# Performance work log

Hardware: AMD Instinct MI355X
Metric: run time of the kernel (lower is better)

The kernel has to match this reference:

```python
import jax, jax.numpy as jnp
import numpy as np

B, NB, H, E, NCT, NL = 16, 4096, 128, 65536, 32, 2
LN_EPS = 1e-5


def _layernorm(x, scale, bias):
    mu = jnp.mean(x, axis=-1, keepdims=True)
    var = jnp.var(x, axis=-1, keepdims=True)
    return (x - mu) / jnp.sqrt(var + LN_EPS) * scale + bias


def setup_inputs() -> dict:
    key = jax.random.key(0)
    ks = jax.random.split(key, 18)
    s = 1.0 / np.sqrt(H)
    inp = {
        'block_tokens': jax.random.normal(ks[0], (B, NB, H), jnp.float32),
        'edge_structure': jnp.full((E,), 0.5, jnp.float32),
        'ct_emb': 0.1 * jax.random.normal(ks[1], (NCT, E), jnp.float32),
        'W_proj': s * jax.random.normal(ks[2], (H, H), jnp.float32),
        'b_proj': jnp.zeros((H,), jnp.float32),
        'W_gate': (1.0 / np.sqrt(2 * H)) * jax.random.normal(ks[3], (2 * H, H), jnp.float32),
        'b_gate': jnp.zeros((H,), jnp.float32),
        'ln_scale': jnp.ones((NL, H), jnp.float32),
        'ln_bias': jnp.zeros((NL, H), jnp.float32),
        'W1': s * jax.random.normal(ks[4], (NL, H, 2 * H), jnp.float32),
        'b1': jnp.zeros((NL, 2 * H), jnp.float32),
        'W2': (1.0 / np.sqrt(2 * H)) * jax.random.normal(ks[5], (NL, 2 * H, H), jnp.float32),
        'b2': jnp.zeros((NL, H), jnp.float32),
        'cancer_type': jax.random.randint(ks[6], (B,), 0, NCT),
        'edge_src': jax.random.randint(ks[7], (E,), 0, NB),
        'edge_dst': jax.random.randint(ks[8], (E,), 0, NB),
        'block_active': jax.random.bernoulli(ks[9], 0.9, (B, NB)),
    }
    return inp


def reference(block_tokens, edge_structure, ct_emb, W_proj, b_proj, W_gate, b_gate,
              ln_scale, ln_bias, W1, b1, W2, b2,
              cancer_type, edge_src, edge_dst, block_active):
    # per-edge signed weights, masked by active src/dst blocks  -> (B, E)
    structure = jax.nn.sigmoid(edge_structure)
    edge_w = structure[None, :] * ct_emb[cancer_type]
    edge_w = edge_w * block_active[:, edge_src].astype(edge_w.dtype) \
                    * block_active[:, edge_dst].astype(edge_w.dtype)
    # route projection + ELU
    h_route = jax.nn.elu(jnp.einsum('bnh,hd->bnd', block_tokens, W_proj) + b_proj)
    # gather sources, weight, scatter-add to destinations
    weighted = edge_w[..., None] * h_route[:, edge_src, :]          # (B, E, H)
    messages = jnp.zeros_like(block_tokens).at[:, edge_dst, :].add(weighted)
    # gated residual
    gate = jax.nn.sigmoid(
        jnp.einsum('bnh,hd->bnd', jnp.concatenate([block_tokens, messages], axis=-1), W_gate) + b_gate)
    x = block_tokens + gate * messages
    # norm + FFN layers (dropout is identity at inference)
    for l in range(NL):
        normed = _layernorm(x, ln_scale[l], ln_bias[l])
        h = jax.nn.elu(jnp.einsum('bnh,hf->bnf', normed, W1[l]) + b1[l])
        x = x + jnp.einsum('bnf,fh->bnh', h, W2[l]) + b2[l]
    return (x, edge_w)
```

## Files before the change

### kernel.cpp

```cpp
#include <hip/hip_runtime.h>
#include <hip/hip_bf16.h>

#define BB     16
#define NBLK   4096
#define HD     128
#define NE     65536
#define MTOT   (BB * NBLK)

typedef __attribute__((ext_vector_type(8))) short bf16x8;
typedef __attribute__((ext_vector_type(4))) float f32x4;

__device__ __forceinline__ float bf2f(unsigned short u) {
    union { unsigned int i; float f; } v; v.i = ((unsigned int)u) << 16; return v.f;
}
__device__ __forceinline__ unsigned short f2bf(float f) {
    __bf16 h = (__bf16)f;
    unsigned short u;
    __builtin_memcpy(&u, &h, 2);
    return u;
}
__device__ __forceinline__ float ldf(const void* p, size_t i, int f32m) {
    return f32m ? ((const float*)p)[i] : bf2f(((const unsigned short*)p)[i]);
}
__device__ __forceinline__ int get_active(const void* p, int i, int mode) {
    switch (mode) {
        case 1:  return ((const unsigned char*)p)[i] != 0;
        case 2:  return ((const unsigned short*)p)[i] != 0;
        case 3:  return ((const float*)p)[i] != 0.f;
        default: return ((const int*)p)[i] != 0;
    }
}
__device__ __forceinline__ float elu_f(float v) {
    const float e = __expf(v);
    return v > 0.f ? v : e - 1.f;
}
__device__ __forceinline__ float sig_f(float v) {
    return 1.f / (1.f + __expf(-v));
}

__global__ void probe_k(const unsigned int* __restrict__ es,
                        const unsigned int* __restrict__ act,
                        int* __restrict__ flags)
{
    const int lane = threadIdx.x;
    const unsigned int v0 = act[lane], v1 = act[64 + lane];
    auto le1  = [](unsigned int v) { return v <= 1u; };
    auto byt  = [](unsigned int v) {
        return ((v & 0xFFu) <= 1u) && (((v >> 8) & 0xFFu) <= 1u) &&
               (((v >> 16) & 0xFFu) <= 1u) && ((v >> 24) <= 1u); };
    auto f32b = [](unsigned int v) { return v == 0u || v == 0x3F800000u; };
    auto bfb  = [](unsigned int v) {
        unsigned short h0 = (unsigned short)(v & 0xFFFFu), h1 = (unsigned short)(v >> 16);
        return (h0 == 0u || h0 == 0x3F80u) && (h1 == 0u || h1 == 0x3F80u); };
    const unsigned long long m_le1 = __ballot(le1(v0) && le1(v1));
    const unsigned long long m_byt = __ballot(byt(v0) && byt(v1));
    const unsigned long long m_f32 = __ballot(f32b(v0) && f32b(v1));
    const unsigned long long m_bf  = __ballot(bfb(v0) && bfb(v1));
    if (lane == 0) {
        flags[0] = (es[0] != 0x3F003F00u) ? 1 : 0;
        const unsigned long long full = ~0ull;
        flags[1] = (m_le1 == full) ? 0
                 : (m_byt == full) ? 1
                 : (m_f32 == full) ? 3
                 : (m_bf  == full) ? 2 : 0;
    }
}

__global__ __launch_bounds__(256) void transpose_k(
    const void* p0, const void* p1, const void* p2, const void* p3,
    const void* p4, const void* p5, unsigned short* __restrict__ wsT,
    const int* __restrict__ flags)
{
    const void* srcs[6]  = {p0, p1, p2, p3, p4, p5};
    const int eoffs[6]   = {0, 0, 0, 32768, 0, 32768};
    const int Ks[6]      = {128, 256, 128, 128, 256, 256};
    const int nsh[6]     = {7,   7,   8,   8,   7,   7};
    const int offs[6]    = {0, 16384, 49152, 81920, 114688, 147456};
    const int f32m = flags[0];
    const int z = blockIdx.y;
    const int K = Ks[z];
    const int Nn = 1 << nsh[z];
    const int idx = blockIdx.x * 256 + threadIdx.x;
    if (idx >= K * Nn) return;
    const int k = idx >> nsh[z];
    const int n = idx & (Nn - 1);
    wsT[offs[z] + n * K + k] = f2bf(ldf(srcs[z], (size_t)eoffs[z] + idx, f32m));
}

__global__ __launch_bounds__(256) void csr_count_k(const int* __restrict__ edst,
                                                   int* __restrict__ cnt)
{
    const int e = blockIdx.x * 256 + threadIdx.x;
    atomicAdd(&cnt[edst[e]], 1);
}

__global__ __launch_bounds__(1024) void csr_scan_k(const int* __restrict__ cnt,
                                                   int* __restrict__ ofs,
                                                   int* __restrict__ cur)
{
    __shared__ int part[1024];
    const int t = threadIdx.x;
    const int4 c = ((const int4*)cnt)[t];
    part[t] = c.x + c.y + c.z + c.w;
    __syncthreads();
    #pragma unroll
    for (int off = 1; off < 1024; off <<= 1) {
        const int v = (t >= off) ? part[t - off] : 0;
        __syncthreads();
        part[t] += v;
        __syncthreads();
    }
    const int base = t ? part[t - 1] : 0;
    int4 o;
    o.x = base; o.y = o.x + c.x; o.z = o.y + c.y; o.w = o.z + c.z;
    ((int4*)ofs)[t] = o;
    ((int4*)cur)[t] = o;
    if (t == 1023) ofs[4096] = part[1023];
}

__global__ __launch_bounds__(256) void csr_fill_k(const int* __restrict__ edst,
                                                  int* __restrict__ cur,
                                                  int* __restrict__ eidx,
                                                  int* __restrict__ pos_e)
{
    const int e = blockIdx.x * 256 + threadIdx.x;
    const int pos = atomicAdd(&cur[edst[e]], 1);
    eidx[pos] = e;
    pos_e[e] = pos;
}

__global__ __launch_bounds__(256) void edge_k(
    const void* __restrict__ es, const void* __restrict__ ctE,
    const int* __restrict__ ctype, const int* __restrict__ esrc, const int* __restrict__ edst,
    const void* __restrict__ act, const int* __restrict__ pos_e,
    float* __restrict__ out_ew, float2* __restrict__ compact,
    const int* __restrict__ flags)
{
    const int f32m = flags[0], am = flags[1];
    const int idx = blockIdx.x * 256 + threadIdx.x;
    const int b = idx >> 16;
    const int e = idx & 65535;
    const int s = esrc[e];
    const float sv  = sig_f(ldf(es, e, f32m));
    const float emb = ldf(ctE, (size_t)ctype[b] * NE + e, f32m);
    const int a1 = get_active(act, b * NBLK + s, am);
    const int a2 = get_active(act, b * NBLK + edst[e], am);
    const float w = (a1 && a2) ? sv * emb : 0.f;
    out_ew[idx] = w;
    compact[((size_t)b << 16) + pos_e[e]] = make_float2(w, __int_as_float(s));
}

__global__ __launch_bounds__(256) void gather_k(
    const float2* __restrict__ compact, const int* __restrict__ ofs,
    const unsigned short* __restrict__ hr, unsigned short* __restrict__ msg)
{
    const int blk = blockIdx.x;
    const int xcd = blk & 7;
    const int i   = blk >> 3;
    const int b   = xcd * 2 + (i & 1);
    const int d   = ((i >> 1) << 2) | (threadIdx.x >> 6);
    const int lane = threadIdx.x & 63;
    const int sub  = lane >> 4;
    const int l15  = lane & 15;
    const int j1 = ofs[d + 1];
    const size_t bbase = (size_t)b * NBLK * HD;
    const float2* cb = compact + ((size_t)b << 16);
    float acc[8];
    #pragma unroll
    for (int i2 = 0; i2 < 8; ++i2) acc[i2] = 0.f;
    int j = ofs[d] + sub;
    float2 c = (j < j1) ? cb[j] : make_float2(0.f, 0.f);
    while (j < j1) {
        const int jn = j + 4;
        const float2 cn = (jn < j1) ? cb[jn] : make_float2(0.f, 0.f);
        if (c.x != 0.f) {
            const int src = __float_as_int(c.y);
            const bf16x8 v = *(const bf16x8*)(hr + bbase + (size_t)src * HD + l15 * 8);
            #pragma unroll
            for (int i2 = 0; i2 < 8; ++i2)
                acc[i2] += c.x * bf2f((unsigned short)v[i2]);
        }
        c = cn; j = jn;
    }
    #pragma unroll
    for (int i2 = 0; i2 < 8; ++i2) {
        acc[i2] += __shfl_xor(acc[i2], 16);
        acc[i2] += __shfl_xor(acc[i2], 32);
    }
    if (sub == 0) {
        bf16x8 o;
        #pragma unroll
        for (int i2 = 0; i2 < 8; ++i2) o[i2] = (short)f2bf(acc[i2]);
        *(bf16x8*)(msg + bbase + (size_t)d * HD + l15 * 8) = o;
    }
}

__global__ __launch_bounds__(256) void route_k(
    const void* __restrict__ bt,
    unsigned short* __restrict__ bt16,
    const unsigned short* __restrict__ WT,
    const void* __restrict__ bias,
    unsigned short* __restrict__ hr,
    const int* __restrict__ flags)
{
    constexpr int K = 128, N = 128, KI = 4, NTW = 2, TILES = 8, NBUF = 4;
    const int f32m = flags[0];
    const int t    = threadIdx.x;
    const int lane = t & 63;
    const int wave = t >> 6;
    const int q    = lane >> 4;
    const int l15  = lane & 15;
    const int n0   = wave * 32;

    {
        const size_t base = (size_t)blockIdx.x * (128 * HD);
        #pragma unroll
        for (int it = 0; it < 8; ++it) {
            const size_t i = base + (size_t)it * 2048 + (size_t)t * 8;
            if (f32m) {
                const float* qp = (const float*)bt + i;
                f32x4 lo = *(const f32x4*)qp;
                f32x4 hi = *(const f32x4*)(qp + 4);
                bf16x8 r;
                #pragma unroll
                for (int j = 0; j < 4; ++j) { r[j] = (short)f2bf(lo[j]); r[4 + j] = (short)f2bf(hi[j]); }
                *(bf16x8*)(bt16 + i) = r;
            } else {
                *(bf16x8*)(bt16 + i) = *(const bf16x8*)((const unsigned short*)bt + i);
            }
        }
    }

    bf16x8 Bf[KI][NTW];
    #pragma unroll
    for (int ki = 0; ki < KI; ++ki)
        #pragma unroll
        for (int nt = 0; nt < NTW; ++nt)
            Bf[ki][nt] = *(const bf16x8*)(WT + (size_t)(n0 + nt * 16 + l15) * K + ki * 32 + q * 8);
    float biasv[NTW];
    #pragma unroll
    for (int nt = 0; nt < NTW; ++nt)
        biasv[nt] = ldf(bias, n0 + nt * 16 + l15, f32m);

    const int tile0 = blockIdx.x * TILES;
    bf16x8 Af[NBUF][KI];
    auto loadA = [&](int tt) {
        const int arow = (tile0 + tt) * 16 + l15;
        if (f32m) {
            const float* ap = (const float*)bt + (size_t)arow * K;
            #pragma unroll
            for (int ki = 0; ki < KI; ++ki) {
                const int k = ki * 32 + q * 8;
                f32x4 a0 = *(const f32x4*)(ap + k);
                f32x4 a1 = *(const f32x4*)(ap + k + 4);
                bf16x8 r;
                #pragma unroll
                for (int j = 0; j < 4; ++j) { r[j] = (short)f2bf(a0[j]); r[4 + j] = (short)f2bf(a1[j]); }
                Af[tt % NBUF][ki] = r;
            }
        } else {
            const unsigned short* ap = (const unsigned short*)bt + (size_t)arow * K;
            #pragma unroll
            for (int ki = 0; ki < KI; ++ki)
                Af[tt % NBUF][ki] = *(const bf16x8*)(ap + ki * 32 + q * 8);
        }
    };
    #pragma unroll
    for (int p = 0; p < NBUF; ++p) loadA(p);

    #pragma unroll
    for (int tt = 0; tt < TILES; ++tt) {
        const int s = tt % NBUF;
        f32x4 acc[NTW];
        #pragma unroll
        for (int i = 0; i < NTW; ++i) acc[i] = (f32x4){0.f, 0.f, 0.f, 0.f};
        #pragma unroll
        for (int ki = 0; ki < KI; ++ki)
            #pragma unroll
            for (int nt = 0; nt < NTW; ++nt)
                acc[nt] = __builtin_amdgcn_mfma_f32_16x16x32_bf16(Af[s][ki], Bf[ki][nt], acc[nt], 0, 0, 0);

        if (tt + NBUF < TILES) loadA(tt + NBUF);

        const int m0 = (tile0 + tt) * 16;
        #pragma unroll
        for (int nt = 0; nt < NTW; ++nt) {
            #pragma unroll
            for (int r = 0; r < 4; ++r) {
                const int row = m0 + q * 4 + r;
                const int col = n0 + nt * 16 + l15;
                const float v = acc[nt][r] + biasv[nt];
                hr[(size_t)row * N + col] = f2bf(elu_f(v));
            }
        }
    }
}

#define XI(xt, row, col)      x_lds[xt][row][((col) + 4 * (row)) & 127]
#define UI(hf, tl, row, col)  U[hf][tl][row][((col) + 8 * (row)) & 255]

__global__ __launch_bounds__(512, 2) void mega_k(
    const unsigned short* __restrict__ bt16,
    const unsigned short* __restrict__ msg,
    const void* __restrict__ btf,
    const unsigned short* __restrict__ WT,
    const void* __restrict__ bg,
    const void* __restrict__ b1, const void* __restrict__ b2,
    const void* __restrict__ lns, const void* __restrict__ lnb,
    float* __restrict__ xout,
    const int* __restrict__ flags)
{
    __shared__ __align__(16) float          x_lds[4][32][128];
    __shared__ __align__(16) unsigned short U[2][2][32][256];

    const int f32m = flags[0];
    const int t    = threadIdx.x;
    const int lane = t & 63;
    const int wave = t >> 6;
    const int hf   = wave >> 2;
    const int wv   = wave & 3;
    const int q    = lane >> 4;
    const int l15  = lane & 15;
    const int rhf  = blockIdx.x * 128 + hf * 64;
    const int ng   = wv * 32;

    float          btv[2][2][2][4];
    unsigned short mgu[2][2][2][4];
    #pragma unroll
    for (int tl = 0; tl < 2; ++tl)
        #pragma unroll
        for (int tt = 0; tt < 2; ++tt)
            #pragma unroll
            for (int nt = 0; nt < 2; ++nt)
                #pragma unroll
                for (int r = 0; r < 4; ++r) {
                    const size_t gi = (size_t)(rhf + tl * 32 + tt * 16 + q * 4 + r) * HD
                                      + ng + nt * 16 + l15;
                    btv[tl][tt][nt][r] = ldf(btf, gi, f32m);
                    mgu[tl][tt][nt][r] = msg[gi];
                }

    const unsigned short* WgT = WT + 16384;

    bf16x8 Bg[8][2];
    #pragma unroll
    for (int ki = 0; ki < 8; ++ki)
        #pragma unroll
        for (int nt = 0; nt < 2; ++nt)
            Bg[ki][nt] = *(const bf16x8*)(WgT + (size_t)(ng + nt * 16 + l15) * 256 + ki * 32 + q * 8);
    float biasg[2];
    #pragma unroll
    for (int nt = 0; nt < 2; ++nt) biasg[nt] = ldf(bg, ng + nt * 16 + l15, f32m);

    #pragma unroll
    for (int tl = 0; tl < 2; ++tl) {
        const int xt = hf * 2 + tl;
        bf16x8 Ag[2][8];
        #pragma unroll
        for (int tt = 0; tt < 2; ++tt) {
            const int arow = rhf + tl * 32 + tt * 16 + l15;
            #pragma unroll
            for (int ki = 0; ki < 8; ++ki) {
                const int k = ki * 32 + q * 8;
                Ag[tt][ki] = (k < HD)
                    ? *(const bf16x8*)(bt16 + (size_t)arow * HD + k)
                    : *(const bf16x8*)(msg  + (size_t)arow * HD + (k - HD));
            }
        }
        #pragma unroll
        for (int tt = 0; tt < 2; ++tt) {
            f32x4 acc[2];
            #pragma unroll
            for (int nt = 0; nt < 2; ++nt) acc[nt] = (f32x4){0.f, 0.f, 0.f, 0.f};
            __builtin_amdgcn_s_setprio(1);
            #pragma unroll
            for (int ki = 0; ki < 8; ++ki)
                #pragma unroll
                for (int nt = 0; nt < 2; ++nt)
                    acc[nt] = __builtin_amdgcn_mfma_f32_16x16x32_bf16(Ag[tt][ki], Bg[ki][nt], acc[nt], 0, 0, 0);
            __builtin_amdgcn_s_setprio(0);
            #pragma unroll
            for (int nt = 0; nt < 2; ++nt)
                #pragma unroll
                for (int r = 0; r < 4; ++r) {
                    const float g = sig_f(acc[nt][r] + biasg[nt]);
                    XI(xt, tt * 16 + q * 4 + r, ng + nt * 16 + l15) =
                        btv[tl][tt][nt][r] + g * bf2f(mgu[tl][tt][nt][r]);
                }
        }
    }
    __syncthreads();

    const int rowln = (t & 255) >> 3;
    const int seg   = t & 7;
    const int n1 = wv * 64;
    const int n2 = wv * 32;

    #pragma unroll
    for (int l = 0; l < 2; ++l) {
        const unsigned short* W1T = WT + (l ? 81920  : 49152);
        const unsigned short* W2T = WT + (l ? 147456 : 114688);
        const long b1o = l ? 256 : 0, b2o = l ? 128 : 0, lno = l ? 128 : 0;

        bf16x8 B1[4][4];
        #pragma unroll
        for (int ki = 0; ki < 4; ++ki)
            #pragma unroll
            for (int nt = 0; nt < 4; ++nt)
                B1[ki][nt] = *(const bf16x8*)(W1T + (size_t)(n1 + nt * 16 + l15) * 128 + ki * 32 + q * 8);
        float bias1[4];
        #pragma unroll
        for (int nt = 0; nt < 4; ++nt) bias1[nt] = ldf(b1, b1o + n1 + nt * 16 + l15, f32m);

        float lsv[16], lbv[16];
        #pragma unroll
        for (int j = 0; j < 4; ++j)
            #pragma unroll
            for (int k = 0; k < 4; ++k) {
                const int col = seg * 16 + j * 4 + k;
                lsv[j * 4 + k] = ldf(lns, lno + col, f32m);
                lbv[j * 4 + k] = ldf(lnb, lno + col, f32m);
            }

        #pragma unroll
        for (int tl = 0; tl < 2; ++tl) {
            const int xt = hf * 2 + tl;
            f32x4 xv[4];
            #pragma unroll
            for (int j = 0; j < 4; ++j)
                xv[j] = *(const f32x4*)&XI(xt, rowln, seg * 16 + j * 4);
            float s = 0.f, ss = 0.f;
            #pragma unroll
            for (int j = 0; j < 4; ++j)
                #pragma unroll
                for (int k = 0; k < 4; ++k) { const float v = xv[j][k]; s += v; ss += v * v; }
            #pragma unroll
            for (int off = 1; off < 8; off <<= 1) { s += __shfl_xor(s, off); ss += __shfl_xor(ss, off); }
            const float mu = s * (1.f / 128.f);
            const float rs = rsqrtf(ss * (1.f / 128.f) - mu * mu + 1e-5f);
            bf16x8 nv[2];
            #pragma unroll
            for (int j = 0; j < 4; ++j)
                #pragma unroll
                for (int k = 0; k < 4; ++k) {
                    const float nn = (xv[j][k] - mu) * rs * lsv[j * 4 + k] + lbv[j * 4 + k];
                    nv[j >> 1][(j & 1) * 4 + k] = (short)f2bf(nn);
                }
            *(bf16x8*)&UI(hf, tl, rowln, seg * 16)     = nv[0];
            *(bf16x8*)&UI(hf, tl, rowln, seg * 16 + 8) = nv[1];
        }
        __syncthreads();

        bf16x8 An[2][2][4];
        #pragma unroll
        for (int tl = 0; tl < 2; ++tl)
            #pragma unroll
            for (int tt = 0; tt < 2; ++tt)
                #pragma unroll
                for (int ki = 0; ki < 4; ++ki)
                    An[tl][tt][ki] = *(const bf16x8*)&UI(hf, tl, tt * 16 + l15, ki * 32 + q * 8);
        __syncthreads();

        #pragma unroll
        for (int tl = 0; tl < 2; ++tl)
            #pragma unroll
            for (int tt = 0; tt < 2; ++tt) {
                f32x4 acc[4];
                #pragma unroll
                for (int nt = 0; nt < 4; ++nt) acc[nt] = (f32x4){0.f, 0.f, 0.f, 0.f};
                __builtin_amdgcn_s_setprio(1);
                #pragma unroll
                for (int ki = 0; ki < 4; ++ki)
                    #pragma unroll
                    for (int nt = 0; nt < 4; ++nt)
                        acc[nt] = __builtin_amdgcn_mfma_f32_16x16x32_bf16(An[tl][tt][ki], B1[ki][nt], acc[nt], 0, 0, 0);
                __builtin_amdgcn_s_setprio(0);
                #pragma unroll
                for (int nt = 0; nt < 4; ++nt)
                    #pragma unroll
                    for (int r = 0; r < 4; ++r)
                        UI(hf, tl, tt * 16 + q * 4 + r, n1 + nt * 16 + l15) =
                            f2bf(elu_f(acc[nt][r] + bias1[nt]));
            }

        bf16x8 B2[8][2];
        #pragma unroll
        for (int ki = 0; ki < 8; ++ki)
            #pragma unroll
            for (int nt = 0; nt < 2; ++nt)
                B2[ki][nt] = *(const bf16x8*)(W2T + (size_t)(n2 + nt * 16 + l15) * 256 + ki * 32 + q * 8);
        float bias2[2];
        #pragma unroll
        for (int nt = 0; nt < 2; ++nt) bias2[nt] = ldf(b2, b2o + n2 + nt * 16 + l15, f32m);
        __syncthreads();

        #pragma unroll
        for (int tl = 0; tl < 2; ++tl) {
            const int xt = hf * 2 + tl;
            #pragma unroll
            for (int tt = 0; tt < 2; ++tt) {
                bf16x8 Ah[8];
                #pragma unroll
                for (int ki = 0; ki < 8; ++ki)
                    Ah[ki] = *(const bf16x8*)&UI(hf, tl, tt * 16 + l15, ki * 32 + q * 8);
                f32x4 acc[2];
                #pragma unroll
                for (int nt = 0; nt < 2; ++nt) acc[nt] = (f32x4){0.f, 0.f, 0.f, 0.f};
                __builtin_amdgcn_s_setprio(1);
                #pragma unroll
                for (int ki = 0; ki < 8; ++ki)
                    #pragma unroll
                    for (int nt = 0; nt < 2; ++nt)
                        acc[nt] = __builtin_amdgcn_mfma_f32_16x16x32_bf16(Ah[ki], B2[ki][nt], acc[nt], 0, 0, 0);
                __builtin_amdgcn_s_setprio(0);
                #pragma unroll
                for (int nt = 0; nt < 2; ++nt)
                    #pragma unroll
                    for (int r = 0; r < 4; ++r)
                        XI(xt, tt * 16 + q * 4 + r, n2 + nt * 16 + l15) += acc[nt][r] + bias2[nt];
            }
        }
        __syncthreads();
    }

    #pragma unroll
    for (int xt = 0; xt < 4; ++xt) {
        float* xo = xout + (size_t)(blockIdx.x * 128 + xt * 32) * HD;
        #pragma unroll
        for (int j = 0; j < 2; ++j) {
            const int idx = j * 512 + t;
            const int r2  = idx >> 5;
            const int c4  = (idx & 31) * 4;
            *(f32x4*)(xo + (size_t)idx * 4) = *(const f32x4*)&XI(xt, r2, c4);
        }
    }
}

extern "C" void kernel_launch(void* const* d_in, const int* in_sizes, int n_in,
                              void* d_out, int out_size, void* d_ws, size_t ws_size,
                              hipStream_t stream)
{
    (void)in_sizes; (void)n_in; (void)out_size; (void)ws_size;

    const void* bt  = d_in[0];
    const void* es  = d_in[1];
    const void* ctE = d_in[2];
    const void* Wp  = d_in[3];
    const void* bp  = d_in[4];
    const void* Wg  = d_in[5];
    const void* bg  = d_in[6];
    const void* lns = d_in[7];
    const void* lnb = d_in[8];
    const void* W1  = d_in[9];
    const void* b1  = d_in[10];
    const void* W2  = d_in[11];
    const void* b2  = d_in[12];
    const int* ctype = (const int*)d_in[13];
    const int* esrc  = (const int*)d_in[14];
    const int* edst  = (const int*)d_in[15];
    const void* act  = d_in[16];

    float* out_x  = (float*)d_out;
    float* out_ew = out_x + (size_t)MTOT * HD;
    float* x = out_x;

    char* ws = (char*)d_ws;
    int*            flags = (int*)ws;
    unsigned short* msg   = (unsigned short*)(ws + 1024);
    unsigned short* bt16  = (unsigned short*)(ws + 1024 + (16ull << 20));
    unsigned short* hr    = (unsigned short*)(ws + 1024 + (32ull << 20));
    char* base48 = ws + 1024 + (48ull << 20);
    int*            cnt     = (int*)(base48);
    int*            ofs     = (int*)(base48 + (16 << 10));
    int*            cur     = (int*)(base48 + (36 << 10));
    int*            eidx    = (int*)(base48 + (52 << 10));
    int*            pos_e   = (int*)(base48 + (308 << 10));
    unsigned short* WT      = (unsigned short*)(base48 + (576 << 10));
    float2*         compact = (float2*)(base48 + (1 << 20));

    const int M = MTOT;

    probe_k<<<1, 64, 0, stream>>>((const unsigned int*)es, (const unsigned int*)act, flags);
    hipMemsetAsync(cnt, 0, NBLK * sizeof(int), stream);

    transpose_k<<<dim3(128, 6), 256, 0, stream>>>(Wp, Wg, W1, W1, W2, W2, WT, flags);

    route_k<<<dim3(M / 128), 256, 0, stream>>>(bt, bt16, WT + 0, bp, hr, flags);

    csr_count_k<<<dim3(NE / 256), 256, 0, stream>>>(edst, cnt);
    csr_scan_k<<<dim3(1), 1024, 0, stream>>>(cnt, ofs, cur);
    csr_fill_k<<<dim3(NE / 256), 256, 0, stream>>>(edst, cur, eidx, pos_e);

    edge_k<<<dim3((BB * NE) / 256), 256, 0, stream>>>(
        es, ctE, ctype, esrc, edst, act, pos_e, out_ew, compact, flags);

    gather_k<<<dim3(M / 4), 256, 0, stream>>>(compact, ofs, hr, msg);

    mega_k<<<dim3(M / 128), 512, 0, stream>>>(
        bt16, msg, bt, WT, bg, b1, b2, lns, lnb, x, flags);
}
```

Measured before the change: 293.7 us.

## Drop bf16 copy of block tokens and unroll gather edge loop by two

route_k no longer writes a bf16 copy of block_tokens. mega_k now reads the original fp32 (or bf16) tokens directly and converts them in registers for the gate GEMM, which removes a 16 MB write and its later read. gather_k processes two edges per iteration with two prefetched compact entries, so more independent row loads are in flight. In exchange, mega_k reads fp32 tokens, twice the bytes of the bf16 copy, and register pressure rises in both kernels.

```diff
diff --git a/kernel.cpp b/kernel.cpp
--- a/kernel.cpp
+++ b/kernel.cpp
@@ -169,18 +169,27 @@
     #pragma unroll
     for (int i2 = 0; i2 < 8; ++i2) acc[i2] = 0.f;
     int j = ofs[d] + sub;
-    float2 c = (j < j1) ? cb[j] : make_float2(0.f, 0.f);
+    float2 c0 = (j     < j1) ? cb[j]     : make_float2(0.f, 0.f);
+    float2 c1 = (j + 4 < j1) ? cb[j + 4] : make_float2(0.f, 0.f);
     while (j < j1) {
-        const int jn = j + 4;
-        const float2 cn = (jn < j1) ? cb[jn] : make_float2(0.f, 0.f);
-        if (c.x != 0.f) {
-            const int src = __float_as_int(c.y);
+        const int jn = j + 8;
+        const float2 n0 = (jn     < j1) ? cb[jn]     : make_float2(0.f, 0.f);
+        const float2 n1 = (jn + 4 < j1) ? cb[jn + 4] : make_float2(0.f, 0.f);
+        if (c0.x != 0.f) {
+            const int src = __float_as_int(c0.y);
             const bf16x8 v = *(const bf16x8*)(hr + bbase + (size_t)src * HD + l15 * 8);
             #pragma unroll
             for (int i2 = 0; i2 < 8; ++i2)
-                acc[i2] += c.x * bf2f((unsigned short)v[i2]);
-        }
-        c = cn; j = jn;
+                acc[i2] += c0.x * bf2f((unsigned short)v[i2]);
+        }
+        if (j + 4 < j1 && c1.x != 0.f) {
+            const int src = __float_as_int(c1.y);
+            const bf16x8 v = *(const bf16x8*)(hr + bbase + (size_t)src * HD + l15 * 8);
+            #pragma unroll
+            for (int i2 = 0; i2 < 8; ++i2)
+                acc[i2] += c1.x * bf2f((unsigned short)v[i2]);
+        }
+        c0 = n0; c1 = n1; j = jn;
     }
     #pragma unroll
     for (int i2 = 0; i2 < 8; ++i2) {
@@ -197,7 +206,6 @@
 
 __global__ __launch_bounds__(256) void route_k(
     const void* __restrict__ bt,
-    unsigned short* __restrict__ bt16,
     const unsigned short* __restrict__ WT,
     const void* __restrict__ bias,
     unsigned short* __restrict__ hr,
@@ -212,25 +220,6 @@
     const int l15  = lane & 15;
     const int n0   = wave * 32;
 
-    {
-        const size_t base = (size_t)blockIdx.x * (128 * HD);
-        #pragma unroll
-        for (int it = 0; it < 8; ++it) {
-            const size_t i = base + (size_t)it * 2048 + (size_t)t * 8;
-            if (f32m) {
-                const float* qp = (const float*)bt + i;
-                f32x4 lo = *(const f32x4*)qp;
-                f32x4 hi = *(const f32x4*)(qp + 4);
-                bf16x8 r;
-                #pragma unroll
-                for (int j = 0; j < 4; ++j) { r[j] = (short)f2bf(lo[j]); r[4 + j] = (short)f2bf(hi[j]); }
-                *(bf16x8*)(bt16 + i) = r;
-            } else {
-                *(bf16x8*)(bt16 + i) = *(const bf16x8*)((const unsigned short*)bt + i);
-            }
-        }
-    }
-
     bf16x8 Bf[KI][NTW];
     #pragma unroll
     for (int ki = 0; ki < KI; ++ki)
@@ -300,7 +289,6 @@
 #define UI(hf, tl, row, col)  U[hf][tl][row][((col) + 8 * (row)) & 255]
 
 __global__ __launch_bounds__(512, 2) void mega_k(
-    const unsigned short* __restrict__ bt16,
     const unsigned short* __restrict__ msg,
     const void* __restrict__ btf,
     const unsigned short* __restrict__ WT,
@@ -359,12 +347,28 @@
         #pragma unroll
         for (int tt = 0; tt < 2; ++tt) {
             const int arow = rhf + tl * 32 + tt * 16 + l15;
-            #pragma unroll
-            for (int ki = 0; ki < 8; ++ki) {
-                const int k = ki * 32 + q * 8;
-                Ag[tt][ki] = (k < HD)
-                    ? *(const bf16x8*)(bt16 + (size_t)arow * HD + k)
-                    : *(const bf16x8*)(msg  + (size_t)arow * HD + (k - HD));
+            if (f32m) {
+                const float* ap = (const float*)btf + (size_t)arow * HD;
+                #pragma unroll
+                for (int ki = 0; ki < 4; ++ki) {
+                    const int k = ki * 32 + q * 8;
+                    f32x4 a0 = *(const f32x4*)(ap + k);
+                    f32x4 a1 = *(const f32x4*)(ap + k + 4);
+                    bf16x8 r;
+                    #pragma unroll
+                    for (int j = 0; j < 4; ++j) { r[j] = (short)f2bf(a0[j]); r[4 + j] = (short)f2bf(a1[j]); }
+                    Ag[tt][ki] = r;
+                }
+            } else {
+                const unsigned short* ap = (const unsigned short*)btf + (size_t)arow * HD;
+                #pragma unroll
+                for (int ki = 0; ki < 4; ++ki)
+                    Ag[tt][ki] = *(const bf16x8*)(ap + ki * 32 + q * 8);
+            }
+            #pragma unroll
+            for (int ki = 4; ki < 8; ++ki) {
+                const int k = ki * 32 + q * 8 - HD;
+                Ag[tt][ki] = *(const bf16x8*)(msg + (size_t)arow * HD + k);
             }
         }
         #pragma unroll
@@ -567,7 +571,6 @@
     char* ws = (char*)d_ws;
     int*            flags = (int*)ws;
     unsigned short* msg   = (unsigned short*)(ws + 1024);
-    unsigned short* bt16  = (unsigned short*)(ws + 1024 + (16ull << 20));
     unsigned short* hr    = (unsigned short*)(ws + 1024 + (32ull << 20));
     char* base48 = ws + 1024 + (48ull << 20);
     int*            cnt     = (int*)(base48);
@@ -585,7 +588,7 @@
 
     transpose_k<<<dim3(128, 6), 256, 0, stream>>>(Wp, Wg, W1, W1, W2, W2, WT, flags);
 
-    route_k<<<dim3(M / 128), 256, 0, stream>>>(bt, bt16, WT + 0, bp, hr, flags);
+    route_k<<<dim3(M / 128), 256, 0, stream>>>(bt, WT + 0, bp, hr, flags);
 
     csr_count_k<<<dim3(NE / 256), 256, 0, stream>>>(edst, cnt);
     csr_scan_k<<<dim3(1), 1024, 0, stream>>>(cnt, ofs, cur);
@@ -597,5 +600,5 @@
     gather_k<<<dim3(M / 4), 256, 0, stream>>>(compact, ofs, hr, msg);
 
     mega_k<<<dim3(M / 128), 512, 0, stream>>>(
-        bt16, msg, bt, WT, bg, b1, b2, lns, lnb, x, flags);
-}
+        msg, bt, WT, bg, b1, b2, lns, lnb, x, flags);
+}
```

After: 297.0 us. No clear change (+1.1%).
